# Kernel optimization log

Measured on AMD Instinct MI355X. Metric: run time of the kernel, lower is better.

## Reference

```python
import jax, jax.numpy as jnp
import numpy as np
from jax import lax

LONG_EDGE = 1024
MAX_SIZE = 1333.0
STRIDES = (4, 8, 16, 32, 64)
SIZES = (32, 64, 128, 256, 512)
RATIOS = (0.5, 1.0, 2.0)
PRE_NMS_TOPK = 6000
POST_NMS_TOPK = 1000
NMS_THRESH = 0.7
NUM_CH = 256


def _gen_anchors_level(scale, ratios, shape, stride):
    # faithful copy of generate_anchors_keras (numpy, static)
    scales, ratios = np.meshgrid(np.array([scale], dtype=np.float64), np.array(ratios, dtype=np.float64))
    scales = scales.flatten(); ratios = ratios.flatten()
    size_ratios = stride * stride / ratios
    widths = np.round(np.sqrt(size_ratios))
    heights = np.round(widths * ratios)
    widths = widths * (scales / stride)
    heights = heights * (scales / stride)
    shifts_y = np.arange(0, shape[0]) * stride + (stride - 1) / 2
    shifts_x = np.arange(0, shape[1]) * stride + (stride - 1) / 2
    shifts_x, shifts_y = np.meshgrid(shifts_x, shifts_y)
    box_widths, box_centers_x = np.meshgrid(widths, shifts_x)
    box_heights, box_centers_y = np.meshgrid(heights, shifts_y)
    box_centers = np.stack([box_centers_y, box_centers_x], axis=2).reshape([-1, 2])
    box_sizes = np.stack([box_heights, box_widths], axis=2).reshape([-1, 2])
    boxes = np.concatenate([box_centers - 0.5 * (box_sizes - 1), box_centers + 0.5 * (box_sizes - 1)], axis=1)
    boxes[:, [2, 3]] += 1
    return boxes[:, [1, 0, 3, 2]].astype(np.float32)


def all_anchors():
    shapes = [(int(np.ceil(LONG_EDGE / s)),) * 2 for s in STRIDES]
    return np.concatenate([_gen_anchors_level(SIZES[i], RATIOS, shapes[i], STRIDES[i]) for i in range(len(STRIDES))], axis=0)


def conv2d(x, w, b, padding):
    y = lax.conv_general_dilated(x, w, (1, 1), padding, dimension_numbers=('NCHW', 'OIHW', 'NCHW'))
    return y + b[None, :, None, None]


def decode_bbox_target(deltas, anchors):
    # deltas, anchors: [K,4]
    txty, twth = deltas[:, :2], deltas[:, 2:]
    x1y1, x2y2 = anchors[:, :2], anchors[:, 2:]
    waha = x2y2 - x1y1
    xaya = (x2y2 + x1y1) * 0.5
    clipv = jnp.float32(np.log(MAX_SIZE / 16.0))
    wbhb = jnp.exp(jnp.minimum(twth, clipv)) * waha
    xbyb = txty * waha + xaya
    return jnp.concatenate([xbyb - wbhb * 0.5, xbyb + wbhb * 0.5], axis=1)


def clip_boxes(b, h, w):
    # faithful to source: x clamped to window[0]=h, y to window[1]=w
    return jnp.stack([b[:, 0].clip(0.0, h), b[:, 1].clip(0.0, w), b[:, 2].clip(0.0, h), b[:, 3].clip(0.0, w)], 1)


def nms_keep(boxes, thresh):
    # boxes sorted by descending score; greedy NMS over full IoU matrix
    x1, y1, x2, y2 = boxes[:, 0], boxes[:, 1], boxes[:, 2], boxes[:, 3]
    areas = (x2 - x1) * (y2 - y1)
    iw = jnp.clip(jnp.minimum(x2[:, None], x2[None, :]) - jnp.maximum(x1[:, None], x1[None, :]), 0.0)
    ih = jnp.clip(jnp.minimum(y2[:, None], y2[None, :]) - jnp.maximum(y1[:, None], y1[None, :]), 0.0)
    inter = iw * ih
    iou = inter / (areas[:, None] + areas[None, :] - inter)
    n = boxes.shape[0]
    sup = iou > thresh
    idxs = jnp.arange(n)
    def body(i, keep):
        row = sup[i] & (idxs > i)
        return jnp.where(keep[i], keep & ~row, keep)
    return lax.fori_loop(0, n, body, jnp.ones((n,), bool))


def rpn_forward(image, feats, w0, b0, wcls, bcls, wbox, bbox):
    labels, boxes_l = [], []
    for f in feats:
        hidden = jax.nn.relu(conv2d(f, w0, b0, 'SAME'))
        cls = conv2d(hidden, wcls, bcls, 'VALID')   # [1,A,H,W]
        box = conv2d(hidden, wbox, bbox, 'VALID')   # [1,4A,H,W]
        labels.append(jnp.transpose(cls, (0, 2, 3, 1)).reshape(1, -1, 1))
        boxes_l.append(jnp.transpose(box, (0, 2, 3, 1)).reshape(1, -1, 4))
    scores = jnp.concatenate(labels, axis=1)[0, :, 0]          # [N]
    box_logits = jnp.concatenate(boxes_l, axis=1)[0]           # [N,4]
    anchors = jnp.asarray(all_anchors())                       # [N,4]
    k = min(PRE_NMS_TOPK, anchors.shape[0])
    _, order = lax.top_k(scores, k)
    deltas = box_logits[order]
    pre_anch = anchors[order]
    dec = decode_bbox_target(deltas, pre_anch)
    h, w = float(image.shape[2]), float(image.shape[3])
    boxes = clip_boxes(dec, h, w)
    keep = nms_keep(lax.stop_gradient(boxes), NMS_THRESH)
    sel = jnp.argsort(~keep)[:POST_NMS_TOPK]  # stable: kept boxes in score order, then pad slots
    proposals = jnp.where(keep[sel][:, None], boxes[sel], 0.0)
    return proposals


def setup_inputs() -> dict:
    key = jax.random.key(0)
    ks = jax.random.split(key, 9)
    hw = [256, 128, 64, 32, 16]
    inp = {'image': jax.random.normal(ks[0], (1, 3, 1024, 1024), jnp.float32)}
    for i, s in enumerate(hw):
        inp[f'feat{i}'] = jax.random.normal(jax.random.fold_in(ks[1], i), (1, NUM_CH, s, s), jnp.float32)
    inp['w0'] = jax.random.normal(ks[2], (NUM_CH, NUM_CH, 3, 3), jnp.float32) * 0.01
    inp['b0'] = jnp.zeros((NUM_CH,), jnp.float32)
    inp['wcls'] = jax.random.normal(ks[3], (3, NUM_CH, 1, 1), jnp.float32) * 0.01
    inp['bcls'] = jnp.zeros((3,), jnp.float32)
    inp['wbox'] = jax.random.normal(ks[4], (12, NUM_CH, 1, 1), jnp.float32) * 0.01
    inp['bbox'] = jnp.zeros((12,), jnp.float32)
    return inp


def reference(image, feat0, feat1, feat2, feat3, feat4, w0, b0, wcls, bcls, wbox, bbox):
    feats = [feat0, feat1, feat2, feat3, feat4]
    return rpn_forward(image, feats, w0, b0, wcls, bcls, wbox, bbox)
```

## Files before the change

kernel.cpp:

```cpp
#include <hip/hip_runtime.h>
#include <cstdint>

typedef unsigned long long u64;
typedef unsigned int u32;
typedef unsigned short ushort;
typedef __attribute__((ext_vector_type(8))) short short8;
typedef __attribute__((ext_vector_type(4))) float f32x4;

#define A_TOTAL 261888
#define NPIX    87296
#define KTOP    6000
#define KTARGET 7800
#define NWORDS  94
#define CANDMAX 8192
#define PIXMAX  8192
#define NBINS   16384

__device__ __forceinline__ u64 score_key64(double s) {
  u64 u = (u64)__double_as_longlong(s);
  return (u & 0x8000000000000000ULL) ? ~u : (u | 0x8000000000000000ULL);
}
__device__ __forceinline__ u32 key32(float s) {
  u32 u = __float_as_uint(s);
  return (u & 0x80000000u) ? ~u : (u | 0x80000000u);
}
__device__ __forceinline__ ushort f2bf(float f) {
  u32 u = __float_as_uint(f);
  u32 r = (u + 0x7FFFu + ((u >> 16) & 1u)) >> 16;
  return (ushort)r;
}
__device__ __forceinline__ void pix_level(int pix, int& l, int& off) {
  if (pix < 65536)      { l = 0; off = 0; }
  else if (pix < 81920) { l = 1; off = 65536; }
  else if (pix < 86016) { l = 2; off = 81920; }
  else if (pix < 87040) { l = 3; off = 86016; }
  else                  { l = 4; off = 87040; }
}

__global__ void k_prep_w(const float* __restrict__ w0, float* __restrict__ wt32,
                         ushort* __restrict__ wkf) {
  int i = blockIdx.x * 256 + threadIdx.x;
  if (i < 256 * 2304) {
    int o = i & 255;
    int ictap = i >> 8;
    float v = w0[o * 2304 + ictap];
    wt32[(size_t)ictap * 256 + o] = v;
    int ic = ictap / 9;
    int tap = ictap - ic * 9;
    int w = o >> 6, mt = (o >> 4) & 3, l15 = o & 15;
    int ch = ic >> 5, kk = ic & 31;
    int l4 = kk >> 3, e = kk & 7;
    int lane = l4 * 16 + l15;
    wkf[((((w * 4 + mt) * 8 + ch) * 9 + tap) << 9) + lane * 8 + e] = f2bf(v);
  }
}

__global__ __launch_bounds__(256, 2) void k_conv_mfma(
    const float* __restrict__ f0, const float* __restrict__ f1,
    const float* __restrict__ f2, const float* __restrict__ f3,
    const float* __restrict__ f4,
    const ushort* __restrict__ wkf, const float* __restrict__ b0,
    const float* __restrict__ wcls, const float* __restrict__ bcls,
    float* __restrict__ scr)
{
  __shared__ ushort xsl[100][40];
  __shared__ float  part[3][64][17];

  int b = blockIdx.x;
  int l, tb;
  if (b < 1024)      { l = 0; tb = b; }
  else if (b < 1280) { l = 1; tb = b - 1024; }
  else if (b < 1344) { l = 2; tb = b - 1280; }
  else if (b < 1360) { l = 3; tb = b - 1344; }
  else               { l = 4; tb = b - 1360; }
  const float* feat = (l == 0) ? f0 : (l == 1) ? f1 : (l == 2) ? f2 : (l == 3) ? f3 : f4;
  int Hh = 256 >> l;
  int HW = Hh * Hh;
  int pixOff = (l == 0) ? 0 : (l == 1) ? 65536 : (l == 2) ? 81920 : (l == 3) ? 86016 : 87040;
  int shl = 5 - l;
  int ty = (tb >> shl) << 3;
  int tx = (tb & ((1 << shl) - 1)) << 3;

  int tid = threadIdx.x;
  int w = tid >> 6;
  int lane = tid & 63;
  int l15 = lane & 15;
  int l4 = lane >> 4;

  f32x4 zz = {0.f, 0.f, 0.f, 0.f};
  f32x4 acc[4][4];
  #pragma unroll
  for (int mt = 0; mt < 4; ++mt)
    #pragma unroll
    for (int tt = 0; tt < 4; ++tt) acc[mt][tt] = zz;

  for (int ch = 0; ch < 8; ++ch) {
    __syncthreads();
    for (int e = tid; e < 3200; e += 256) {
      int icl = e / 100;
      int sp = e - icl * 100;
      int yy = sp / 10;
      int xx = sp - yy * 10;
      int gy = ty + yy - 1, gx = tx + xx - 1;
      float v = 0.f;
      if (gy >= 0 && gy < Hh && gx >= 0 && gx < Hh)
        v = feat[(ch * 32 + icl) * HW + gy * Hh + gx];
      xsl[sp][icl] = f2bf(v);
    }
    __syncthreads();
    #pragma unroll
    for (int tap = 0; tap < 9; ++tap) {
      int dy = tap / 3;
      int dx = tap - dy * 3;
      short8 af[4], bf[4];
      #pragma unroll
      for (int mt = 0; mt < 4; ++mt) {
        int abase = ((((w * 4 + mt) * 8 + ch) * 9 + tap) << 9) + (lane << 3);
        af[mt] = *(const short8*)(wkf + abase);
      }
      #pragma unroll
      for (int tt = 0; tt < 4; ++tt) {
        int p = (tt << 4) + l15;
        int sp = ((p >> 3) + dy) * 10 + (p & 7) + dx;
        bf[tt] = *(const short8*)&xsl[sp][l4 << 3];
      }
      #pragma unroll
      for (int mt = 0; mt < 4; ++mt)
        #pragma unroll
        for (int tt = 0; tt < 4; ++tt)
          acc[mt][tt] = __builtin_amdgcn_mfma_f32_16x16x32_bf16(af[mt], bf[tt], acc[mt][tt], 0, 0, 0);
    }
  }

  float pr[3][4];
  #pragma unroll
  for (int kk = 0; kk < 3; ++kk)
    #pragma unroll
    for (int tt = 0; tt < 4; ++tt) pr[kk][tt] = 0.f;
  #pragma unroll
  for (int mt = 0; mt < 4; ++mt) {
    #pragma unroll
    for (int r = 0; r < 4; ++r) {
      int oc = (w << 6) + (mt << 4) + (l4 << 2) + r;
      float bb = b0[oc];
      float c0 = wcls[oc], c1 = wcls[256 + oc], c2 = wcls[512 + oc];
      #pragma unroll
      for (int tt = 0; tt < 4; ++tt) {
        float v = acc[mt][tt][r] + bb;
        v = v > 0.f ? v : 0.f;
        pr[0][tt] = fmaf(c0, v, pr[0][tt]);
        pr[1][tt] = fmaf(c1, v, pr[1][tt]);
        pr[2][tt] = fmaf(c2, v, pr[2][tt]);
      }
    }
  }
  __syncthreads();
  #pragma unroll
  for (int kk = 0; kk < 3; ++kk)
    #pragma unroll
    for (int tt = 0; tt < 4; ++tt)
      part[kk][(tt << 4) + l15][(w << 2) + l4] = pr[kk][tt];
  __syncthreads();
  if (tid < 192) {
    int kk = tid >> 6;
    int px = tid & 63;
    float s = 0.f;
    #pragma unroll
    for (int q = 0; q < 16; ++q) s += part[kk][px][q];
    int pix = pixOff + (ty + (px >> 3)) * Hh + (tx + (px & 7));
    scr[pix * 3 + kk] = s + bcls[kk];
  }
}

__global__ void k_hist1(const float* __restrict__ scr, u32* __restrict__ bins) {
  __shared__ u32 h[NBINS];
  int tid = threadIdx.x;
  for (int idx = tid; idx < NBINS; idx += 256) h[idx] = 0;
  __syncthreads();
  for (int i = blockIdx.x * 256 + tid; i < A_TOTAL; i += gridDim.x * 256)
    atomicAdd(&h[key32(scr[i]) >> 18], 1u);
  __syncthreads();
  for (int idx = tid; idx < NBINS; idx += 256) {
    u32 v = h[idx];
    if (v) atomicAdd(&bins[idx], v);
  }
}

__global__ void k_scan1(const u32* __restrict__ bins, u32* __restrict__ meta) {
  __shared__ u32 psum[256];
  int tid = threadIdx.x;
  u32 s = 0;
  for (int u = 0; u < 64; ++u) s += bins[tid * 64 + u];
  psum[tid] = s;
  __syncthreads();
  if (tid == 0) {
    u32 run = 0;
    for (int t = 255; t >= 0; --t) { u32 tmp = psum[t]; psum[t] = run; run += tmp; }
  }
  __syncthreads();
  u32 cum = psum[tid];
  if (cum < (u32)KTARGET) {
    for (int u = 63; u >= 0; --u) {
      u32 bv = bins[tid * 64 + u];
      u32 nc = cum + bv;
      if (nc >= (u32)KTARGET) {
        meta[0] = (u32)(tid * 64 + u);
        meta[2] = cum;
        break;
      }
      cum = nc;
    }
  }
}

__global__ void k_hist2(const float* __restrict__ scr, const u32* __restrict__ meta,
                        u32* __restrict__ sub) {
  int i = blockIdx.x * 256 + threadIdx.x;
  if (i < A_TOTAL) {
    u32 k = key32(scr[i]);
    if ((k >> 18) == meta[0]) atomicAdd(&sub[(k >> 10) & 0xFFu], 1u);
  }
}

__global__ void k_scan2(const u32* __restrict__ sub, u32* __restrict__ meta) {
  if (threadIdx.x == 0) {
    u32 b = meta[0];
    u32 c = meta[2];
    u32 T = b << 18;
    for (int u = 255; u >= 0; --u) {
      c += sub[u];
      if (c >= (u32)KTARGET) { T = (b << 18) | ((u32)u << 10); break; }
    }
    meta[3] = (T >= (2u << 10)) ? (T - (2u << 10)) : 0u;
  }
}

__global__ void k_cnt2(const float* __restrict__ scr, const u32* __restrict__ meta,
                       u32* __restrict__ blkCnt, u32* __restrict__ blkCntP) {
  __shared__ u32 wc[4], wcp[4];
  int tid = threadIdx.x;
  int lane = tid & 63, wv = tid >> 6;
  u32 T = meta[3];
  int i = blockIdx.x * 256 + tid;
  bool qa = (i < A_TOTAL) && (key32(scr[i]) >= T);
  u64 ba = __ballot(qa);
  bool qp = false;
  if (i < NPIX)
    qp = (key32(scr[i * 3 + 0]) >= T) || (key32(scr[i * 3 + 1]) >= T) || (key32(scr[i * 3 + 2]) >= T);
  u64 bp = __ballot(qp);
  if (lane == 0) { wc[wv] = (u32)__popcll(ba); wcp[wv] = (u32)__popcll(bp); }
  __syncthreads();
  if (tid == 0) {
    blkCnt[blockIdx.x]  = wc[0] + wc[1] + wc[2] + wc[3];
    blkCntP[blockIdx.x] = wcp[0] + wcp[1] + wcp[2] + wcp[3];
  }
}

__global__ __launch_bounds__(1024) void k_scanblk2(const u32* __restrict__ blkCnt,
                                                   u32* __restrict__ blkOff,
                                                   u32* __restrict__ totA,
                                                   const u32* __restrict__ blkCntP,
                                                   u32* __restrict__ blkOffP,
                                                   u32* __restrict__ totP) {
  __shared__ u32 buf[2][1024];
  int tid = threadIdx.x;
  for (int pass = 0; pass < 2; ++pass) {
    const u32* src_ = pass ? blkCntP : blkCnt;
    u32* dst_ = pass ? blkOffP : blkOff;
    u32* tot_ = pass ? totP : totA;
    u32 v = (tid < 1023) ? src_[tid] : 0u;
    buf[0][tid] = v;
    __syncthreads();
    int src = 0;
    for (int d = 1; d < 1024; d <<= 1) {
      u32 t = buf[src][tid] + ((tid >= d) ? buf[src][tid - d] : 0u);
      buf[src ^ 1][tid] = t;
      src ^= 1;
      __syncthreads();
    }
    if (tid < 1023) dst_[tid] = buf[src][tid] - v;
    if (tid == 0) tot_[0] = buf[src][1022];
    __syncthreads();
  }
}

__global__ void k_fill2(const float* __restrict__ scr, const u32* __restrict__ meta,
                        const u32* __restrict__ blkOff, const u32* __restrict__ blkOffP,
                        u32* __restrict__ candIdx, u32* __restrict__ pixList,
                        u32* __restrict__ pixMap) {
  __shared__ u32 wbase[4], wbaseP[4];
  int tid = threadIdx.x;
  int lane = tid & 63, wv = tid >> 6;
  u32 T = meta[3];
  int i = blockIdx.x * 256 + tid;
  bool qa = (i < A_TOTAL) && (key32(scr[i]) >= T);
  u64 ba = __ballot(qa);
  bool qp = false;
  if (i < NPIX)
    qp = (key32(scr[i * 3 + 0]) >= T) || (key32(scr[i * 3 + 1]) >= T) || (key32(scr[i * 3 + 2]) >= T);
  u64 bp = __ballot(qp);
  if (lane == 0) { wbase[wv] = (u32)__popcll(ba); wbaseP[wv] = (u32)__popcll(bp); }
  __syncthreads();
  if (tid == 0) {
    u32 r = blkOff[blockIdx.x];
    #pragma unroll
    for (int w2 = 0; w2 < 4; ++w2) { u32 t = wbase[w2]; wbase[w2] = r; r += t; }
    u32 rp = blkOffP[blockIdx.x];
    #pragma unroll
    for (int w2 = 0; w2 < 4; ++w2) { u32 t = wbaseP[w2]; wbaseP[w2] = rp; rp += t; }
  }
  __syncthreads();
  if (qa) {
    u32 rank = (u32)__popcll(ba & ((1ULL << lane) - 1ULL));
    u32 pos = wbase[wv] + rank;
    if (pos < CANDMAX) candIdx[pos] = (u32)i;
  }
  if (qp) {
    u32 rank = (u32)__popcll(bp & ((1ULL << lane) - 1ULL));
    u32 pos = wbaseP[wv] + rank;
    if (pos < PIXMAX) { pixList[pos] = (u32)i; pixMap[i] = pos; }
  }
}

#define KCH 144
__global__ __launch_bounds__(256, 6) void k_hidden(
    const float* __restrict__ f0, const float* __restrict__ f1,
    const float* __restrict__ f2, const float* __restrict__ f3,
    const float* __restrict__ f4,
    const float* __restrict__ wt32,
    const u32* __restrict__ pixList, const u32* __restrict__ meta,
    double* __restrict__ hpart)
{
  __shared__ float patch[2][KCH][16];
  __shared__ int sValid[16], sY[16], sX[16], sW[16], sL[16];

  int tid = threadIdx.x;
  int pixblk = blockIdx.x >> 2;
  int kc = blockIdx.x & 3;
  int base = pixblk * 16;
  u32 np = meta[4];
  if (np > PIXMAX) np = PIXMAX;
  if (base >= (int)np) return;

  if (tid < 16) {
    int slot = base + tid;
    int v = slot < (int)np;
    sValid[tid] = v;
    int pix = v ? (int)pixList[slot] : 0;
    int l, off;
    pix_level(pix, l, off);
    int W = 256 >> l;
    int idx = pix - off;
    sL[tid] = l;
    sW[tid] = W;
    sY[tid] = idx >> (8 - l);
    sX[tid] = idx & (W - 1);
  }
  __syncthreads();

  auto stage = [&](int cb, int pb) {
    for (int t = tid; t < 768; t += 256) {
      int s = t & 15;
      int rem = t >> 4;
      int icl = rem / 3;
      int dy = rem - icl * 3;
      int ic = cb * 16 + icl;
      float v0 = 0.f, v1 = 0.f, v2 = 0.f;
      if (sValid[s]) {
        int l = sL[s], W = sW[s], y = sY[s], x = sX[s];
        const float* feat = (l == 0) ? f0 : (l == 1) ? f1 : (l == 2) ? f2 : (l == 3) ? f3 : f4;
        int gy = y + dy - 1;
        if (gy >= 0 && gy < W) {
          const float* rowp = feat + ic * W * W + gy * W;
          if (x - 1 >= 0) v0 = rowp[x - 1];
          v1 = rowp[x];
          if (x + 1 < W) v2 = rowp[x + 1];
        }
      }
      int kb = icl * 9 + dy * 3;
      patch[pb][kb + 0][s] = v0;
      patch[pb][kb + 1][s] = v1;
      patch[pb][kb + 2][s] = v2;
    }
  };

  int ocq = tid & 63;
  int pxq = tid >> 6;

  double acc[4][4];
  #pragma unroll
  for (int i = 0; i < 4; ++i)
    #pragma unroll
    for (int j = 0; j < 4; ++j) acc[i][j] = 0.0;

  int cb0 = kc * 4;
  stage(cb0, 0);
  __syncthreads();

  for (int i = 0; i < 4; ++i) {
    int cb = cb0 + i;
    if (i < 3) stage(cb + 1, (i + 1) & 1);
    const float (*pc)[16] = patch[i & 1];
    const float* wb_ = wt32 + (size_t)(cb * KCH) * 256 + (ocq << 2);
    for (int kk = 0; kk < KCH; ++kk) {
      float4 p4 = *(const float4*)&pc[kk][pxq << 2];
      double pd0 = (double)p4.x, pd1 = (double)p4.y;
      double pd2 = (double)p4.z, pd3 = (double)p4.w;
      float4 wf = *(const float4*)(wb_ + (size_t)kk * 256);
      double w0_ = (double)wf.x, w1_ = (double)wf.y;
      double w2_ = (double)wf.z, w3_ = (double)wf.w;
      acc[0][0] = fma(w0_, pd0, acc[0][0]);
      acc[0][1] = fma(w0_, pd1, acc[0][1]);
      acc[0][2] = fma(w0_, pd2, acc[0][2]);
      acc[0][3] = fma(w0_, pd3, acc[0][3]);
      acc[1][0] = fma(w1_, pd0, acc[1][0]);
      acc[1][1] = fma(w1_, pd1, acc[1][1]);
      acc[1][2] = fma(w1_, pd2, acc[1][2]);
      acc[1][3] = fma(w1_, pd3, acc[1][3]);
      acc[2][0] = fma(w2_, pd0, acc[2][0]);
      acc[2][1] = fma(w2_, pd1, acc[2][1]);
      acc[2][2] = fma(w2_, pd2, acc[2][2]);
      acc[2][3] = fma(w2_, pd3, acc[2][3]);
      acc[3][0] = fma(w3_, pd0, acc[3][0]);
      acc[3][1] = fma(w3_, pd1, acc[3][1]);
      acc[3][2] = fma(w3_, pd2, acc[3][2]);
      acc[3][3] = fma(w3_, pd3, acc[3][3]);
    }
    __syncthreads();
  }

  #pragma unroll
  for (int j = 0; j < 4; ++j) {
    int s = (pxq << 2) + j;
    if (sValid[s]) {
      double* dst = &hpart[((size_t)kc * PIXMAX + base + s) * 256 + (ocq << 2)];
      dst[0] = acc[0][j];
      dst[1] = acc[1][j];
      dst[2] = acc[2][j];
      dst[3] = acc[3][j];
    }
  }
}

__global__ __launch_bounds__(256, 4) void k_heads(
    const float* __restrict__ wcls, const float* __restrict__ bcls,
    const float* __restrict__ wbox, const float* __restrict__ bbox,
    const float* __restrict__ b0,
    const u32* __restrict__ candIdx, const u32* __restrict__ pixMap,
    const u32* __restrict__ meta, const double* __restrict__ hpart,
    u64* __restrict__ candKey, u32* __restrict__ candPack, double* __restrict__ candDelta)
{
  __shared__ double wavePart[8][5][4];
  __shared__ int sIdx[8], sValid[8], sR[8], sPS[8];
  int tid = threadIdx.x;
  int lane = tid & 63;
  int wv = tid >> 6;
  int base = blockIdx.x * 8;
  u32 cnt = meta[1];
  if (cnt > CANDMAX) cnt = CANDMAX;

  if (base >= (int)cnt) {
    if (tid < 8) {
      candKey[base + tid] = 0ULL;
      candPack[base + tid] = 0xFFFFFFFFu;
    }
    return;
  }

  if (tid < 8) {
    int slot = base + tid;
    int v = slot < (int)cnt;
    sValid[tid] = v;
    int aidx = v ? (int)candIdx[slot] : 0;
    sIdx[tid] = aidx;
    int pix = aidx / 3;
    sR[tid] = aidx - pix * 3;
    sPS[tid] = v ? (int)pixMap[pix] : 0;
  }
  __syncthreads();

  double bb = (double)b0[tid];
  for (int s = 0; s < 8; ++s) {
    if (!sValid[s]) continue;
    int r = sR[s];
    size_t ps = (size_t)sPS[s];
    double hv = hpart[ps * 256 + tid];
    hv = hv + hpart[((size_t)PIXMAX + ps) * 256 + tid];
    hv = hv + hpart[((size_t)2 * PIXMAX + ps) * 256 + tid];
    hv = hv + hpart[((size_t)3 * PIXMAX + ps) * 256 + tid];
    hv = hv + bb;
    hv = hv > 0.0 ? hv : 0.0;
    double p0 = (double)wcls[r * 256 + tid] * hv;
    double p1 = (double)wbox[(r * 4 + 0) * 256 + tid] * hv;
    double p2 = (double)wbox[(r * 4 + 1) * 256 + tid] * hv;
    double p3 = (double)wbox[(r * 4 + 2) * 256 + tid] * hv;
    double p4 = (double)wbox[(r * 4 + 3) * 256 + tid] * hv;
    #pragma unroll
    for (int d = 32; d; d >>= 1) {
      p0 += __shfl_xor(p0, d);
      p1 += __shfl_xor(p1, d);
      p2 += __shfl_xor(p2, d);
      p3 += __shfl_xor(p3, d);
      p4 += __shfl_xor(p4, d);
    }
    if (lane == 0) {
      wavePart[s][0][wv] = p0;
      wavePart[s][1][wv] = p1;
      wavePart[s][2][wv] = p2;
      wavePart[s][3][wv] = p3;
      wavePart[s][4][wv] = p4;
    }
  }
  __syncthreads();
  if (tid < 40) {
    int s = tid / 5;
    int k = tid - s * 5;
    int slot = base + s;
    if (sValid[s]) {
      double v = wavePart[s][k][0] + wavePart[s][k][1] + wavePart[s][k][2] + wavePart[s][k][3];
      int r = sR[s];
      if (k == 0) {
        double sc_ = v + (double)bcls[r];
        candKey[slot] = score_key64(sc_);
        candPack[slot] = ((u32)sIdx[s] << 13) | (u32)slot;
      } else {
        candDelta[(size_t)slot * 4 + (k - 1)] = v + (double)bbox[r * 4 + (k - 1)];
      }
    } else if (k == 0) {
      candKey[slot] = 0ULL;
      candPack[slot] = 0xFFFFFFFFu;
    }
  }
}

__global__ __launch_bounds__(256) void k_rank(const u64* __restrict__ candKey,
                                              const u32* __restrict__ candPack,
                                              u32* __restrict__ order) {
  __shared__ u64 fk[1024];
  __shared__ u32 fp[1024];
  __shared__ u32 rsum[32][8];
  int tid = threadIdx.x;
  int c = tid & 31;
  int g = tid >> 5;
  int ci = blockIdx.x * 32 + c;
  u64 mk = candKey[ci];
  u32 mp = candPack[ci];
  u32 cnt = 0;
  for (int chunk = 0; chunk < 8; ++chunk) {
    __syncthreads();
    for (int e = tid; e < 1024; e += 256) {
      fk[e] = candKey[chunk * 1024 + e];
      fp[e] = candPack[chunk * 1024 + e];
    }
    __syncthreads();
    int j0 = g * 128;
    #pragma unroll 4
    for (int j = j0; j < j0 + 128; ++j) {
      u64 kj = fk[j];
      cnt += (kj > mk || (kj == mk && fp[j] < mp)) ? 1u : 0u;
    }
  }
  rsum[c][g] = cnt;
  __syncthreads();
  if (tid < 32) {
    u32 rank = 0;
    #pragma unroll
    for (int q = 0; q < 8; ++q) rank += rsum[tid][q];
    if (rank < (u32)KTOP) order[rank] = mp;
  }
}

__global__ void k_decode(const u32* __restrict__ order, const double* __restrict__ candDelta,
                         double* __restrict__ boxesD) {
  int i = blockIdx.x * 64 + threadIdx.x;
  if (i >= KTOP) return;
  u32 pack = order[i];
  u32 slot = pack & 0x1FFFu;
  u32 a = pack >> 13;
  int pix = (int)(a / 3u);
  int r = (int)(a - (u32)pix * 3u);
  int l, off;
  pix_level(pix, l, off);
  int W = 256 >> l;
  int idx = pix - off;
  int y = idx >> (8 - l);
  int x = idx & (W - 1);
  int s = 4 << l;
  double ratio = (r == 0) ? 0.5 : (r == 1) ? 1.0 : 2.0;
  double wq = rint(sqrt((double)(s * s) / ratio));
  double hq = rint(wq * ratio);
  double Wa = wq * 8.0, Ha = hq * 8.0;
  double cx = (double)x * (double)s + (double)(s - 1) * 0.5;
  double cy = (double)y * (double)s + (double)(s - 1) * 0.5;
  double ax1 = (double)(float)(cx - 0.5 * (Wa - 1.0));
  double ay1 = (double)(float)(cy - 0.5 * (Ha - 1.0));
  double ax2 = (double)(float)(cx + 0.5 * (Wa - 1.0) + 1.0);
  double ay2 = (double)(float)(cy + 0.5 * (Ha - 1.0) + 1.0);
  double tx = candDelta[(size_t)slot * 4 + 0], tyv = candDelta[(size_t)slot * 4 + 1];
  double tw = candDelta[(size_t)slot * 4 + 2], th  = candDelta[(size_t)slot * 4 + 3];
  double wa = ax2 - ax1, ha = ay2 - ay1;
  double xa = (ax1 + ax2) * 0.5, ya = (ay1 + ay2) * 0.5;
  double clipv = (double)(float)log(1333.0 / 16.0);
  double wb = exp(fmin(tw, clipv)) * wa;
  double hb = exp(fmin(th, clipv)) * ha;
  double xb = tx * wa + xa;
  double yb = tyv * ha + ya;
  double bx1 = xb - 0.5 * wb, by1 = yb - 0.5 * hb;
  double bx2 = xb + 0.5 * wb, by2 = yb + 0.5 * hb;
  bx1 = fmin(fmax(bx1, 0.0), 1024.0);
  by1 = fmin(fmax(by1, 0.0), 1024.0);
  bx2 = fmin(fmax(bx2, 0.0), 1024.0);
  by2 = fmin(fmax(by2, 0.0), 1024.0);
  boxesD[(size_t)i * 4 + 0] = bx1;
  boxesD[(size_t)i * 4 + 1] = by1;
  boxesD[(size_t)i * 4 + 2] = bx2;
  boxesD[(size_t)i * 4 + 3] = by2;
}

__global__ void k_mask(const double* __restrict__ boxesD, u64* __restrict__ maskA) {
  __shared__ double cbx[64][4];
  int lane = threadIdx.x;
  int bc = blockIdx.x, br = blockIdx.y;
  if (bc < br) return;
  int ci = bc * 64 + lane;
  if (ci < KTOP) {
    cbx[lane][0] = boxesD[(size_t)ci * 4 + 0];
    cbx[lane][1] = boxesD[(size_t)ci * 4 + 1];
    cbx[lane][2] = boxesD[(size_t)ci * 4 + 2];
    cbx[lane][3] = boxesD[(size_t)ci * 4 + 3];
  } else {
    cbx[lane][0] = -1e30; cbx[lane][1] = -1e30; cbx[lane][2] = -1e30; cbx[lane][3] = -1e30;
  }
  __syncthreads();
  int ri = br * 64 + lane;
  if (ri >= KTOP) return;
  double rx1 = boxesD[(size_t)ri * 4 + 0], ry1 = boxesD[(size_t)ri * 4 + 1];
  double rx2 = boxesD[(size_t)ri * 4 + 2], ry2 = boxesD[(size_t)ri * 4 + 3];
  double ra = (rx2 - rx1) * (ry2 - ry1);
  u64 bits = 0;
  #pragma unroll 4
  for (int j = 0; j < 64; ++j) {
    int cj = bc * 64 + j;
    double iw = fmin(rx2, cbx[j][2]) - fmax(rx1, cbx[j][0]);
    double ih = fmin(ry2, cbx[j][3]) - fmax(ry1, cbx[j][1]);
    iw = fmax(iw, 0.0); ih = fmax(ih, 0.0);
    double inter = iw * ih;
    double ca = (cbx[j][2] - cbx[j][0]) * (cbx[j][3] - cbx[j][1]);
    double iou = inter / (ra + ca - inter);
    if (cj > ri && iou > 0.7) bits |= (1ULL << j);
  }
  maskA[(size_t)ri * NWORDS + bc] = bits;
}

__global__ __launch_bounds__(1024) void k_nms_reduce(const u64* __restrict__ maskA,
                                                     u32* __restrict__ keep) {
  __shared__ u64 rm[NWORDS];
  int tid = threadIdx.x;
  int wv = tid >> 6, lane = tid & 63;
  for (int i = tid; i < NWORDS; i += 1024) rm[i] = 0ULL;
  __syncthreads();
  u64 diagNext = maskA[(size_t)lane * NWORDS + 0];
  int keptTot = 0;
  for (int c = 0; c < NWORDS; ++c) {
    int rows = KTOP - c * 64; if (rows > 64) rows = 64;
    u64 validM = (rows == 64) ? ~0ULL : ((1ULL << rows) - 1ULL);
    size_t rowbase = (size_t)(c * 64 + lane) * NWORDS;
    bool lv = lane < rows;
    int w0i = c + wv;
    u64 v0 = (lv && w0i      < NWORDS) ? maskA[rowbase + w0i]      : 0ULL;
    u64 v1 = (lv && w0i + 16 < NWORDS) ? maskA[rowbase + w0i + 16] : 0ULL;
    u64 v2 = (lv && w0i + 32 < NWORDS) ? maskA[rowbase + w0i + 32] : 0ULL;
    u64 v3 = (lv && w0i + 48 < NWORDS) ? maskA[rowbase + w0i + 48] : 0ULL;
    u64 v4 = (lv && w0i + 64 < NWORDS) ? maskA[rowbase + w0i + 64] : 0ULL;
    u64 v5 = (lv && w0i + 80 < NWORDS) ? maskA[rowbase + w0i + 80] : 0ULL;
    u64 diag = diagNext;
    if (c + 1 < NWORDS) {
      int nrows = KTOP - (c + 1) * 64; if (nrows > 64) nrows = 64;
      diagNext = (lane < nrows) ? maskA[(size_t)((c + 1) * 64 + lane) * NWORDS + (c + 1)] : 0ULL;
    }
    u64 R = rm[c];
    u64 undec = (~R) & validM;
    u64 km = 0;
    while (undec) {
      int j = __builtin_ctzll(undec);
      km |= (1ULL << j);
      u64 dj = (u64)__shfl((unsigned long long)diag, j);
      undec &= ~(dj | (1ULL << j));
    }
    if (wv == 0 && lane < rows) keep[c * 64 + lane] = (u32)((km >> lane) & 1ULL);
    keptTot += (int)__popcll(km);
    if (keptTot >= 1000) {
      for (int i = (c + 1) * 64 + tid; i < KTOP; i += 1024) keep[i] = 0u;
      return;
    }
    u64 sel = ((km >> lane) & 1ULL) ? ~0ULL : 0ULL;
    v0 &= sel; v1 &= sel; v2 &= sel; v3 &= sel; v4 &= sel; v5 &= sel;
    #pragma unroll
    for (int s = 32; s; s >>= 1) {
      v0 |= (u64)__shfl_xor((unsigned long long)v0, s);
      v1 |= (u64)__shfl_xor((unsigned long long)v1, s);
      v2 |= (u64)__shfl_xor((unsigned long long)v2, s);
      v3 |= (u64)__shfl_xor((unsigned long long)v3, s);
      v4 |= (u64)__shfl_xor((unsigned long long)v4, s);
      v5 |= (u64)__shfl_xor((unsigned long long)v5, s);
    }
    if (lane == 0) {
      if (w0i      < NWORDS) rm[w0i]      |= v0;
      if (w0i + 16 < NWORDS) rm[w0i + 16] |= v1;
      if (w0i + 32 < NWORDS) rm[w0i + 32] |= v2;
      if (w0i + 48 < NWORDS) rm[w0i + 48] |= v3;
      if (w0i + 64 < NWORDS) rm[w0i + 64] |= v4;
      if (w0i + 80 < NWORDS) rm[w0i + 80] |= v5;
    }
    __syncthreads();
  }
}

__global__ __launch_bounds__(1024) void k_emit(const u32* __restrict__ keep,
                                               const double* __restrict__ boxesD,
                                               float* __restrict__ out) {
  __shared__ u32 partial[1024];
  __shared__ u32 excl[1024];
  int tid = threadIdx.x;
  for (int j = tid; j < 4000; j += 1024) out[j] = 0.f;
  int base = tid * 6;
  u32 kv[6];
  u32 c = 0;
  #pragma unroll
  for (int u = 0; u < 6; ++u) {
    int j = base + u;
    kv[u] = (j < KTOP) ? keep[j] : 0u;
    c += kv[u];
  }
  partial[tid] = c;
  __syncthreads();
  if (tid == 0) {
    u32 run = 0;
    for (int t = 0; t < 1024; ++t) { excl[t] = run; run += partial[t]; }
  }
  __syncthreads();
  u32 p = excl[tid];
  #pragma unroll
  for (int u = 0; u < 6; ++u) {
    int j = base + u;
    if (j < KTOP && kv[u]) {
      if (p < 1000u) {
        out[p * 4 + 0] = (float)boxesD[(size_t)j * 4 + 0];
        out[p * 4 + 1] = (float)boxesD[(size_t)j * 4 + 1];
        out[p * 4 + 2] = (float)boxesD[(size_t)j * 4 + 2];
        out[p * 4 + 3] = (float)boxesD[(size_t)j * 4 + 3];
      }
      ++p;
    }
  }
}

extern "C" void kernel_launch(void* const* d_in, const int* in_sizes, int n_in,
                              void* d_out, int out_size, void* d_ws, size_t ws_size,
                              hipStream_t stream) {
  const float* f0   = (const float*)d_in[1];
  const float* f1   = (const float*)d_in[2];
  const float* f2   = (const float*)d_in[3];
  const float* f3   = (const float*)d_in[4];
  const float* f4   = (const float*)d_in[5];
  const float* w0   = (const float*)d_in[6];
  const float* b0   = (const float*)d_in[7];
  const float* wcls = (const float*)d_in[8];
  const float* bcls = (const float*)d_in[9];
  const float* wbox = (const float*)d_in[10];
  const float* bbox = (const float*)d_in[11];
  float* out = (float*)d_out;
  char* ws = (char*)d_ws;

  size_t off = 0;
  auto alloc = [&](size_t bytes) { size_t o = off; off += (bytes + 255) & ~(size_t)255; return o; };
  size_t off_scr  = alloc((size_t)A_TOTAL * 4);
  size_t off_wt   = alloc((size_t)256 * 2304 * 4);
  size_t off_wk   = alloc((size_t)256 * 2304 * 2);
  size_t off_hp   = alloc((size_t)4 * PIXMAX * 256 * 8);
  size_t off_ci   = alloc((size_t)CANDMAX * 4);
  size_t off_ck   = alloc((size_t)CANDMAX * 8);
  size_t off_cp   = alloc((size_t)CANDMAX * 4);
  size_t off_cd   = alloc((size_t)CANDMAX * 4 * 8);
  size_t off_pl   = alloc((size_t)PIXMAX * 4);
  size_t off_pm   = alloc((size_t)NPIX * 4);
  size_t off_box  = alloc((size_t)KTOP * 4 * 8);
  size_t off_ord  = alloc((size_t)KTOP * 4);
  size_t off_keep = alloc((size_t)KTOP * 4);
  size_t off_mask = alloc((size_t)KTOP * NWORDS * 8);
  size_t off_bcnt = alloc((size_t)1024 * 4);
  size_t off_boff = alloc((size_t)1024 * 4);
  size_t off_bcp  = alloc((size_t)1024 * 4);
  size_t off_bop  = alloc((size_t)1024 * 4);
  size_t off_bins = alloc((size_t)NBINS * 4);
  size_t off_sub  = alloc((size_t)256 * 4);
  size_t off_meta = alloc((size_t)64 * 4);
  size_t off_end  = off;
  (void)in_sizes; (void)n_in; (void)out_size; (void)ws_size;

  float*  scr       = (float*)(ws + off_scr);
  float*  wt32      = (float*)(ws + off_wt);
  ushort* wkf       = (ushort*)(ws + off_wk);
  double* hpart     = (double*)(ws + off_hp);
  u32*    candIdx   = (u32*)(ws + off_ci);
  u64*    candKey   = (u64*)(ws + off_ck);
  u32*    candPack  = (u32*)(ws + off_cp);
  double* candDelta = (double*)(ws + off_cd);
  u32*    pixList   = (u32*)(ws + off_pl);
  u32*    pixMap    = (u32*)(ws + off_pm);
  double* boxesD    = (double*)(ws + off_box);
  u32*    order     = (u32*)(ws + off_ord);
  u32*    keep      = (u32*)(ws + off_keep);
  u64*    maskA     = (u64*)(ws + off_mask);
  u32*    blkCnt    = (u32*)(ws + off_bcnt);
  u32*    blkOff    = (u32*)(ws + off_boff);
  u32*    blkCntP   = (u32*)(ws + off_bcp);
  u32*    blkOffP   = (u32*)(ws + off_bop);
  u32*    bins      = (u32*)(ws + off_bins);
  u32*    sub       = (u32*)(ws + off_sub);
  u32*    meta      = (u32*)(ws + off_meta);

  hipMemsetAsync(ws + off_bins, 0, off_end - off_bins, stream);

  k_prep_w<<<2304, 256, 0, stream>>>(w0, wt32, wkf);
  k_conv_mfma<<<1364, 256, 0, stream>>>(f0, f1, f2, f3, f4, wkf, b0, wcls, bcls, scr);
  k_hist1<<<64, 256, 0, stream>>>(scr, bins);
  k_scan1<<<1, 256, 0, stream>>>(bins, meta);
  k_hist2<<<1023, 256, 0, stream>>>(scr, meta, sub);
  k_scan2<<<1, 64, 0, stream>>>(sub, meta);
  k_cnt2<<<1023, 256, 0, stream>>>(scr, meta, blkCnt, blkCntP);
  k_scanblk2<<<1, 1024, 0, stream>>>(blkCnt, blkOff, meta + 1, blkCntP, blkOffP, meta + 4);
  k_fill2<<<1023, 256, 0, stream>>>(scr, meta, blkOff, blkOffP, candIdx, pixList, pixMap);
  k_hidden<<<(PIXMAX / 16) * 4, 256, 0, stream>>>(f0, f1, f2, f3, f4, wt32, pixList, meta, hpart);
  k_heads<<<CANDMAX / 8, 256, 0, stream>>>(wcls, bcls, wbox, bbox, b0, candIdx, pixMap, meta,
                                           hpart, candKey, candPack, candDelta);
  k_rank<<<CANDMAX / 32, 256, 0, stream>>>(candKey, candPack, order);
  k_decode<<<94, 64, 0, stream>>>(order, candDelta, boxesD);
  k_mask<<<dim3(NWORDS, NWORDS), 64, 0, stream>>>(boxesD, maskA);
  k_nms_reduce<<<1, 1024, 0, stream>>>(maskA, keep);
  k_emit<<<1, 1024, 0, stream>>>(keep, boxesD, out);
}
```

Baseline: 928.8 us.

## Double-buffer conv and hidden staging via registers, fuse decode into rank

The MFMA conv kernel now prefetches the next channel chunk's input patch into registers while the current chunk's MFMAs run, then commits it to a second LDS buffer. Its final cross-wave reduction is replaced by wave shuffles plus a smaller LDS array, and the launch-bounds occupancy hint rises from 2 to 3. k_hidden gets the same register-prefetch split, an unroll pragma and a lower occupancy hint. The separate decode kernel is folded into k_rank, which removes one launch and the order buffer. The 13-float register prefetch raises register pressure, which could cause spills under the higher occupancy target.

```diff
diff --git a/kernel.cpp b/kernel.cpp
--- a/kernel.cpp
+++ b/kernel.cpp
@@ -55,7 +55,7 @@
   }
 }
 
-__global__ __launch_bounds__(256, 2) void k_conv_mfma(
+__global__ __launch_bounds__(256, 3) void k_conv_mfma(
     const float* __restrict__ f0, const float* __restrict__ f1,
     const float* __restrict__ f2, const float* __restrict__ f3,
     const float* __restrict__ f4,
@@ -63,8 +63,8 @@
     const float* __restrict__ wcls, const float* __restrict__ bcls,
     float* __restrict__ scr)
 {
-  __shared__ ushort xsl[100][40];
-  __shared__ float  part[3][64][17];
+  __shared__ ushort xsl[2][100][40];
+  __shared__ float  partW[3][4][16][4];
 
   int b = blockIdx.x;
   int l, tb;
@@ -94,20 +94,43 @@
     #pragma unroll
     for (int tt = 0; tt < 4; ++tt) acc[mt][tt] = zz;
 
+  float rv[13];
+  auto stageLoad = [&](int ch) {
+    #pragma unroll
+    for (int n = 0; n < 13; ++n) {
+      int e = tid + n * 256;
+      float v = 0.f;
+      if (e < 3200) {
+        int icl = e / 100;
+        int sp = e - icl * 100;
+        int yy = sp / 10;
+        int xx = sp - yy * 10;
+        int gy = ty + yy - 1, gx = tx + xx - 1;
+        if (gy >= 0 && gy < Hh && gx >= 0 && gx < Hh)
+          v = feat[(ch * 32 + icl) * HW + gy * Hh + gx];
+      }
+      rv[n] = v;
+    }
+  };
+  auto stageCommit = [&](int pb) {
+    #pragma unroll
+    for (int n = 0; n < 13; ++n) {
+      int e = tid + n * 256;
+      if (e < 3200) {
+        int icl = e / 100;
+        int sp = e - icl * 100;
+        xsl[pb][sp][icl] = f2bf(rv[n]);
+      }
+    }
+  };
+
+  stageLoad(0);
+  stageCommit(0);
+  __syncthreads();
+
   for (int ch = 0; ch < 8; ++ch) {
-    __syncthreads();
-    for (int e = tid; e < 3200; e += 256) {
-      int icl = e / 100;
-      int sp = e - icl * 100;
-      int yy = sp / 10;
-      int xx = sp - yy * 10;
-      int gy = ty + yy - 1, gx = tx + xx - 1;
-      float v = 0.f;
-      if (gy >= 0 && gy < Hh && gx >= 0 && gx < Hh)
-        v = feat[(ch * 32 + icl) * HW + gy * Hh + gx];
-      xsl[sp][icl] = f2bf(v);
-    }
-    __syncthreads();
+    if (ch < 7) stageLoad(ch + 1);
+    const ushort (*xc)[40] = xsl[ch & 1];
     #pragma unroll
     for (int tap = 0; tap < 9; ++tap) {
       int dy = tap / 3;
@@ -122,7 +145,7 @@
       for (int tt = 0; tt < 4; ++tt) {
         int p = (tt << 4) + l15;
         int sp = ((p >> 3) + dy) * 10 + (p & 7) + dx;
-        bf[tt] = *(const short8*)&xsl[sp][l4 << 3];
+        bf[tt] = *(const short8*)&xc[sp][l4 << 3];
       }
       #pragma unroll
       for (int mt = 0; mt < 4; ++mt)
@@ -130,6 +153,8 @@
         for (int tt = 0; tt < 4; ++tt)
           acc[mt][tt] = __builtin_amdgcn_mfma_f32_16x16x32_bf16(af[mt], bf[tt], acc[mt][tt], 0, 0, 0);
     }
+    if (ch < 7) stageCommit((ch + 1) & 1);
+    __syncthreads();
   }
 
   float pr[3][4];
@@ -154,19 +179,29 @@
       }
     }
   }
-  __syncthreads();
   #pragma unroll
   for (int kk = 0; kk < 3; ++kk)
     #pragma unroll
-    for (int tt = 0; tt < 4; ++tt)
-      part[kk][(tt << 4) + l15][(w << 2) + l4] = pr[kk][tt];
+    for (int tt = 0; tt < 4; ++tt) {
+      float v = pr[kk][tt];
+      v += __shfl_xor(v, 16);
+      v += __shfl_xor(v, 32);
+      pr[kk][tt] = v;
+    }
+  if (l4 == 0) {
+    #pragma unroll
+    for (int kk = 0; kk < 3; ++kk)
+      #pragma unroll
+      for (int tt = 0; tt < 4; ++tt)
+        partW[kk][tt][l15][w] = pr[kk][tt];
+  }
   __syncthreads();
   if (tid < 192) {
     int kk = tid >> 6;
     int px = tid & 63;
-    float s = 0.f;
-    #pragma unroll
-    for (int q = 0; q < 16; ++q) s += part[kk][px][q];
+    int tt = px >> 4, li = px & 15;
+    float s = partW[kk][tt][li][0] + partW[kk][tt][li][1] +
+              partW[kk][tt][li][2] + partW[kk][tt][li][3];
     int pix = pixOff + (ty + (px >> 3)) * Hh + (tx + (px & 7));
     scr[pix * 3 + kk] = s + bcls[kk];
   }
@@ -323,7 +358,7 @@
 }
 
 #define KCH 144
-__global__ __launch_bounds__(256, 6) void k_hidden(
+__global__ __launch_bounds__(256, 4) void k_hidden(
     const float* __restrict__ f0, const float* __restrict__ f1,
     const float* __restrict__ f2, const float* __restrict__ f3,
     const float* __restrict__ f4,
@@ -358,8 +393,11 @@
   }
   __syncthreads();
 
-  auto stage = [&](int cb, int pb) {
-    for (int t = tid; t < 768; t += 256) {
+  float rv[3][3];
+  auto stageLoad = [&](int cb) {
+    #pragma unroll
+    for (int n = 0; n < 3; ++n) {
+      int t = tid + n * 256;
       int s = t & 15;
       int rem = t >> 4;
       int icl = rem / 3;
@@ -377,10 +415,21 @@
           if (x + 1 < W) v2 = rowp[x + 1];
         }
       }
+      rv[n][0] = v0; rv[n][1] = v1; rv[n][2] = v2;
+    }
+  };
+  auto stageCommit = [&](int pb) {
+    #pragma unroll
+    for (int n = 0; n < 3; ++n) {
+      int t = tid + n * 256;
+      int s = t & 15;
+      int rem = t >> 4;
+      int icl = rem / 3;
+      int dy = rem - icl * 3;
       int kb = icl * 9 + dy * 3;
-      patch[pb][kb + 0][s] = v0;
-      patch[pb][kb + 1][s] = v1;
-      patch[pb][kb + 2][s] = v2;
+      patch[pb][kb + 0][s] = rv[n][0];
+      patch[pb][kb + 1][s] = rv[n][1];
+      patch[pb][kb + 2][s] = rv[n][2];
     }
   };
 
@@ -394,14 +443,16 @@
     for (int j = 0; j < 4; ++j) acc[i][j] = 0.0;
 
   int cb0 = kc * 4;
-  stage(cb0, 0);
+  stageLoad(cb0);
+  stageCommit(0);
   __syncthreads();
 
   for (int i = 0; i < 4; ++i) {
     int cb = cb0 + i;
-    if (i < 3) stage(cb + 1, (i + 1) & 1);
+    if (i < 3) stageLoad(cb + 1);
     const float (*pc)[16] = patch[i & 1];
     const float* wb_ = wt32 + (size_t)(cb * KCH) * 256 + (ocq << 2);
+    #pragma unroll 4
     for (int kk = 0; kk < KCH; ++kk) {
       float4 p4 = *(const float4*)&pc[kk][pxq << 2];
       double pd0 = (double)p4.x, pd1 = (double)p4.y;
@@ -426,6 +477,7 @@
       acc[3][2] = fma(w3_, pd2, acc[3][2]);
       acc[3][3] = fma(w3_, pd3, acc[3][3]);
     }
+    if (i < 3) stageCommit((i + 1) & 1);
     __syncthreads();
   }
 
@@ -535,7 +587,8 @@
 
 __global__ __launch_bounds__(256) void k_rank(const u64* __restrict__ candKey,
                                               const u32* __restrict__ candPack,
-                                              u32* __restrict__ order) {
+                                              const double* __restrict__ candDelta,
+                                              double* __restrict__ boxesD) {
   __shared__ u64 fk[1024];
   __shared__ u32 fp[1024];
   __shared__ u32 rsum[32][8];
@@ -566,55 +619,50 @@
     u32 rank = 0;
     #pragma unroll
     for (int q = 0; q < 8; ++q) rank += rsum[tid][q];
-    if (rank < (u32)KTOP) order[rank] = mp;
-  }
-}
-
-__global__ void k_decode(const u32* __restrict__ order, const double* __restrict__ candDelta,
-                         double* __restrict__ boxesD) {
-  int i = blockIdx.x * 64 + threadIdx.x;
-  if (i >= KTOP) return;
-  u32 pack = order[i];
-  u32 slot = pack & 0x1FFFu;
-  u32 a = pack >> 13;
-  int pix = (int)(a / 3u);
-  int r = (int)(a - (u32)pix * 3u);
-  int l, off;
-  pix_level(pix, l, off);
-  int W = 256 >> l;
-  int idx = pix - off;
-  int y = idx >> (8 - l);
-  int x = idx & (W - 1);
-  int s = 4 << l;
-  double ratio = (r == 0) ? 0.5 : (r == 1) ? 1.0 : 2.0;
-  double wq = rint(sqrt((double)(s * s) / ratio));
-  double hq = rint(wq * ratio);
-  double Wa = wq * 8.0, Ha = hq * 8.0;
-  double cx = (double)x * (double)s + (double)(s - 1) * 0.5;
-  double cy = (double)y * (double)s + (double)(s - 1) * 0.5;
-  double ax1 = (double)(float)(cx - 0.5 * (Wa - 1.0));
-  double ay1 = (double)(float)(cy - 0.5 * (Ha - 1.0));
-  double ax2 = (double)(float)(cx + 0.5 * (Wa - 1.0) + 1.0);
-  double ay2 = (double)(float)(cy + 0.5 * (Ha - 1.0) + 1.0);
-  double tx = candDelta[(size_t)slot * 4 + 0], tyv = candDelta[(size_t)slot * 4 + 1];
-  double tw = candDelta[(size_t)slot * 4 + 2], th  = candDelta[(size_t)slot * 4 + 3];
-  double wa = ax2 - ax1, ha = ay2 - ay1;
-  double xa = (ax1 + ax2) * 0.5, ya = (ay1 + ay2) * 0.5;
-  double clipv = (double)(float)log(1333.0 / 16.0);
-  double wb = exp(fmin(tw, clipv)) * wa;
-  double hb = exp(fmin(th, clipv)) * ha;
-  double xb = tx * wa + xa;
-  double yb = tyv * ha + ya;
-  double bx1 = xb - 0.5 * wb, by1 = yb - 0.5 * hb;
-  double bx2 = xb + 0.5 * wb, by2 = yb + 0.5 * hb;
-  bx1 = fmin(fmax(bx1, 0.0), 1024.0);
-  by1 = fmin(fmax(by1, 0.0), 1024.0);
-  bx2 = fmin(fmax(bx2, 0.0), 1024.0);
-  by2 = fmin(fmax(by2, 0.0), 1024.0);
-  boxesD[(size_t)i * 4 + 0] = bx1;
-  boxesD[(size_t)i * 4 + 1] = by1;
-  boxesD[(size_t)i * 4 + 2] = bx2;
-  boxesD[(size_t)i * 4 + 3] = by2;
+    if (rank < (u32)KTOP) {
+      u32 pack = mp;
+      u32 slot = pack & 0x1FFFu;
+      u32 a = pack >> 13;
+      int pix = (int)(a / 3u);
+      int r = (int)(a - (u32)pix * 3u);
+      int l, off;
+      pix_level(pix, l, off);
+      int W = 256 >> l;
+      int idx = pix - off;
+      int y = idx >> (8 - l);
+      int x = idx & (W - 1);
+      int sst = 4 << l;
+      double ratio = (r == 0) ? 0.5 : (r == 1) ? 1.0 : 2.0;
+      double wq = rint(sqrt((double)(sst * sst) / ratio));
+      double hq = rint(wq * ratio);
+      double Wa = wq * 8.0, Ha = hq * 8.0;
+      double cx = (double)x * (double)sst + (double)(sst - 1) * 0.5;
+      double cy = (double)y * (double)sst + (double)(sst - 1) * 0.5;
+      double ax1 = (double)(float)(cx - 0.5 * (Wa - 1.0));
+      double ay1 = (double)(float)(cy - 0.5 * (Ha - 1.0));
+      double ax2 = (double)(float)(cx + 0.5 * (Wa - 1.0) + 1.0);
+      double ay2 = (double)(float)(cy + 0.5 * (Ha - 1.0) + 1.0);
+      double tx = candDelta[(size_t)slot * 4 + 0], tyv = candDelta[(size_t)slot * 4 + 1];
+      double tw = candDelta[(size_t)slot * 4 + 2], th  = candDelta[(size_t)slot * 4 + 3];
+      double wa = ax2 - ax1, ha = ay2 - ay1;
+      double xa = (ax1 + ax2) * 0.5, ya = (ay1 + ay2) * 0.5;
+      double clipv = (double)(float)log(1333.0 / 16.0);
+      double wb = exp(fmin(tw, clipv)) * wa;
+      double hb = exp(fmin(th, clipv)) * ha;
+      double xb = tx * wa + xa;
+      double yb = tyv * ha + ya;
+      double bx1 = xb - 0.5 * wb, by1 = yb - 0.5 * hb;
+      double bx2 = xb + 0.5 * wb, by2 = yb + 0.5 * hb;
+      bx1 = fmin(fmax(bx1, 0.0), 1024.0);
+      by1 = fmin(fmax(by1, 0.0), 1024.0);
+      bx2 = fmin(fmax(bx2, 0.0), 1024.0);
+      by2 = fmin(fmax(by2, 0.0), 1024.0);
+      boxesD[(size_t)rank * 4 + 0] = bx1;
+      boxesD[(size_t)rank * 4 + 1] = by1;
+      boxesD[(size_t)rank * 4 + 2] = bx2;
+      boxesD[(size_t)rank * 4 + 3] = by2;
+    }
+  }
 }
 
 __global__ void k_mask(const double* __restrict__ boxesD, u64* __restrict__ maskA) {
@@ -785,7 +833,6 @@
   size_t off_pl   = alloc((size_t)PIXMAX * 4);
   size_t off_pm   = alloc((size_t)NPIX * 4);
   size_t off_box  = alloc((size_t)KTOP * 4 * 8);
-  size_t off_ord  = alloc((size_t)KTOP * 4);
   size_t off_keep = alloc((size_t)KTOP * 4);
   size_t off_mask = alloc((size_t)KTOP * NWORDS * 8);
   size_t off_bcnt = alloc((size_t)1024 * 4);
@@ -809,7 +856,6 @@
   u32*    pixList   = (u32*)(ws + off_pl);
   u32*    pixMap    = (u32*)(ws + off_pm);
   double* boxesD    = (double*)(ws + off_box);
-  u32*    order     = (u32*)(ws + off_ord);
   u32*    keep      = (u32*)(ws + off_keep);
   u64*    maskA     = (u64*)(ws + off_mask);
   u32*    blkCnt    = (u32*)(ws + off_bcnt);
@@ -834,8 +880,7 @@
   k_hidden<<<(PIXMAX / 16) * 4, 256, 0, stream>>>(f0, f1, f2, f3, f4, wt32, pixList, meta, hpart);
   k_heads<<<CANDMAX / 8, 256, 0, stream>>>(wcls, bcls, wbox, bbox, b0, candIdx, pixMap, meta,
                                            hpart, candKey, candPack, candDelta);
-  k_rank<<<CANDMAX / 32, 256, 0, stream>>>(candKey, candPack, order);
-  k_decode<<<94, 64, 0, stream>>>(order, candDelta, boxesD);
+  k_rank<<<CANDMAX / 32, 256, 0, stream>>>(candKey, candPack, candDelta, boxesD);
   k_mask<<<dim3(NWORDS, NWORDS), 64, 0, stream>>>(boxesD, maskA);
   k_nms_reduce<<<1, 1024, 0, stream>>>(maskA, keep);
   k_emit<<<1, 1024, 0, stream>>>(keep, boxesD, out);
```

Measured after the change: 1.111 ms. +19.7%, slower.
